# Optimization experiments

Measured on AMD Instinct MI355X. Metric: run time of the kernel, lower is better.

The kernel has to match this reference:

```python
import jax, jax.numpy as jnp
import numpy as np

B, C, HW, NP, L, D, NH, OUT = 32, 3, 224, 14, 12, 768, 12, 1000
PS = HW // NP            # 16
IN_D = C * PS * PS       # 768
S = NP * NP + 1          # 197
DH = D // NH             # 64
MD = 4 * D               # 3072


def setup_inputs() -> dict:
    key = jax.random.key(0)
    ks = iter(jax.random.split(key, 32))
    g = lambda shape: jax.random.normal(next(ks), shape, dtype=jnp.float32) * 0.02
    return {
        "images": jax.random.normal(next(ks), (B, C, HW, HW), dtype=jnp.float32),
        "Wp": g((D, IN_D)), "bp": jnp.zeros((D,), jnp.float32),
        "cls": jax.random.normal(next(ks), (1, D), dtype=jnp.float32),
        "pos": jnp.zeros((S, D), jnp.float32),  # frozen zeros in original
        "ln1_g": jnp.ones((L, D), jnp.float32), "ln1_b": jnp.zeros((L, D), jnp.float32),
        "Wq": g((L, NH, DH, DH)), "bq": jnp.zeros((L, NH, DH), jnp.float32),
        "Wk": g((L, NH, DH, DH)), "bk": jnp.zeros((L, NH, DH), jnp.float32),
        "Wv": g((L, NH, DH, DH)), "bv": jnp.zeros((L, NH, DH), jnp.float32),
        "ln2_g": jnp.ones((L, D), jnp.float32), "ln2_b": jnp.zeros((L, D), jnp.float32),
        "W1": g((L, MD, D)), "b1": jnp.zeros((L, MD), jnp.float32),
        "W2": g((L, D, MD)), "b2": jnp.zeros((L, D), jnp.float32),
        "Wh": g((OUT, D)), "bh": jnp.zeros((OUT,), jnp.float32),
    }


def _layernorm(x, g, b, eps=1e-5):
    m = jnp.mean(x, axis=-1, keepdims=True)
    v = jnp.var(x, axis=-1, keepdims=True)
    return (x - m) * jax.lax.rsqrt(v + eps) * g + b


def reference(images, Wp, bp, cls, pos, ln1_g, ln1_b, Wq, bq, Wk, bk, Wv, bv,
              ln2_g, ln2_b, W1, b1, W2, b2, Wh, bh):
    n = images.shape[0]
    # patchify: flatten order is (c, ph, pw) per patch, matching torch .flatten()
    p = images.reshape(n, C, NP, PS, NP, PS).transpose(0, 2, 4, 1, 3, 5)
    p = p.reshape(n, NP * NP, IN_D)
    tokens = p @ Wp.T + bp                                    # [B, NP^2, D]
    tokens = jnp.concatenate([jnp.broadcast_to(cls, (n, 1, D)), tokens], axis=1)
    x = tokens + pos                                          # [B, S, D]

    scale = 1.0 / np.sqrt(DH)

    def block(x, prm):
        g1, b1n, wq, bqv, wk, bkv, wv, bvv, g2, b2n, w1, b1v, w2, b2v = prm
        h = _layernorm(x, g1, b1n)
        hh = h.reshape(n, S, NH, DH)                          # split heads
        q = jnp.einsum('bshd,hed->bshe', hh, wq) + bqv
        k = jnp.einsum('bshd,hed->bshe', hh, wk) + bkv
        v = jnp.einsum('bshd,hed->bshe', hh, wv) + bvv
        att = jax.nn.softmax(jnp.einsum('bqhe,bkhe->bhqk', q, k) * scale, axis=-1)
        o = jnp.einsum('bhqk,bkhe->bqhe', att, v).reshape(n, S, D)
        x = x + o
        h2 = _layernorm(x, g2, b2n)
        m = jax.nn.gelu(h2 @ w1.T + b1v, approximate=False) @ w2.T + b2v
        return x + m, None

    x, _ = jax.lax.scan(block, x,
                        (ln1_g, ln1_b, Wq, bq, Wk, bk, Wv, bv,
                         ln2_g, ln2_b, W1, b1, W2, b2))
    logits = x[:, 0] @ Wh.T + bh
    return jax.nn.softmax(logits, axis=-1)
```

## Files before the change

kernel.cpp:

```cpp
#include <hip/hip_runtime.h>
#include <math.h>
#include <stdint.h>

#define NBATCH 32
#define SEQ 197
#define DIM 768
#define NHEAD 12
#define DH 64
#define MDIM 3072
#define NLAYER 12
#define NPATCH 196
#define NOUT 1000
#define MROWS (NBATCH * SEQ)
#define SPLITK 2

typedef __bf16 bf16x8 __attribute__((ext_vector_type(8)));
typedef float f32x4 __attribute__((ext_vector_type(4)));

__device__ __forceinline__ unsigned short f2bf(float f) {
    unsigned u = __float_as_uint(f);
    unsigned r = u + 0x7fffu + ((u >> 16) & 1u);
    return (unsigned short)(r >> 16);
}

__device__ __forceinline__ f32x4 mfma16(bf16x8 a, bf16x8 b, f32x4 c) {
    return __builtin_amdgcn_mfma_f32_16x16x32_bf16(a, b, c, 0, 0, 0);
}

__device__ __forceinline__ void gload_lds16(const void* g, const void* lds) {
    __builtin_amdgcn_global_load_lds(
        (const __attribute__((address_space(1))) void*)(uintptr_t)g,
        (__attribute__((address_space(3))) void*)(uint32_t)(uintptr_t)lds,
        16, 0, 0);
}

#define WAIT_VMCNT_4() asm volatile("s_waitcnt vmcnt(4)" ::: "memory")
#define WAIT_VMCNT_0() asm volatile("s_waitcnt vmcnt(0)" ::: "memory")
#define BARRIER_RAW()                      \
    do {                                   \
        asm volatile("" ::: "memory");     \
        __builtin_amdgcn_s_barrier();      \
        asm volatile("" ::: "memory");     \
    } while (0)

__global__ __launch_bounds__(256) void cvt4(const float* __restrict__ src,
                                            unsigned short* __restrict__ dst, int n4) {
    int stride = gridDim.x * 256;
    for (int i = blockIdx.x * 256 + threadIdx.x; i < n4; i += stride) {
        float4 f = *(const float4*)(src + (size_t)i * 4);
        ushort4 o;
        o.x = f2bf(f.x); o.y = f2bf(f.y); o.z = f2bf(f.z); o.w = f2bf(f.w);
        *(ushort4*)(dst + (size_t)i * 4) = o;
    }
}

__global__ __launch_bounds__(256) void cvt_qkvw(const float* __restrict__ Wq,
                                                const float* __restrict__ Wk,
                                                const float* __restrict__ Wv,
                                                unsigned short* __restrict__ dst) {
    const int n = NLAYER * NHEAD * 3 * 64 * 64;
    int stride = gridDim.x * 256;
    for (int i = blockIdx.x * 256 + threadIdx.x; i < n; i += stride) {
        int d = i & 63, e = (i >> 6) & 63;
        int v = i >> 12;
        int t = v % 3, hh = (v / 3) % NHEAD, l = v / (3 * NHEAD);
        const float* src = (t == 0) ? Wq : (t == 1) ? Wk : Wv;
        dst[i] = f2bf(src[(((size_t)(l * NHEAD + hh)) * 64 + e) * 64 + d]);
    }
}

__global__ __launch_bounds__(256) void cls_pos_kernel(const float* __restrict__ cls,
                                                      const float* __restrict__ pos,
                                                      float* __restrict__ x) {
    int b = blockIdx.x, tid = threadIdx.x;
#pragma unroll
    for (int i = 0; i < 3; i++) {
        int c = tid + i * 256;
        x[(size_t)b * SEQ * DIM + c] = cls[c] + pos[c];
    }
}

__global__ __launch_bounds__(256) void gemm_patch_bf(const unsigned short* __restrict__ imgbf,
                                                     const unsigned short* __restrict__ wpbf,
                                                     const float* __restrict__ bp,
                                                     const float* __restrict__ pos,
                                                     float* __restrict__ x) {
    __shared__ __align__(16) unsigned short As[2][128 * 32];
    __shared__ __align__(16) unsigned short Bs[2][128 * 32];
    const int t = threadIdx.x, l = t & 63, w = t >> 6;
    const int bm = blockIdx.x * 128, bn = blockIdx.y * 128;
    const int wr = w >> 1, wc = w & 1;
    f32x4 acc[4][4] = {};

    const int ra0 = t >> 2, ka0 = (t & 3) * 8;
    const int ra1 = (t + 256) >> 2, ka1 = ((t + 256) & 3) * 8;
    int gm0 = bm + ra0, b0 = gm0 / NPATCH, p0 = gm0 % NPATCH;
    int gm1 = bm + ra1, b1 = gm1 / NPATCH, p1 = gm1 % NPATCH;
    const unsigned short* ib0 =
        imgbf + ((size_t)b0 * 3 * 224 + (size_t)(p0 / 14) * 16) * 224 + (p0 % 14) * 16;
    const unsigned short* ib1 =
        imgbf + ((size_t)b1 * 3 * 224 + (size_t)(p1 / 14) * 16) * 224 + (p1 % 14) * 16;
    const unsigned short* Br0 = wpbf + (size_t)(bn + ra0) * 768 + ka0;
    const unsigned short* Br1 = wpbf + (size_t)(bn + ra1) * 768 + ka1;
    const int lA0 = (0 * 256 + w * 64) * 8, lA1 = (1 * 256 + w * 64) * 8;
    const int lr = l & 15, lk = (l >> 4) * 8;

#define PATCH_STAGE(buf, k0)                                                   \
    {                                                                          \
        int kA0 = (k0) + ka0, kA1 = (k0) + ka1;                                \
        int c0 = kA0 >> 8, i0 = (kA0 >> 4) & 15, j0 = kA0 & 15;                \
        int c1 = kA1 >> 8, i1 = (kA1 >> 4) & 15, j1 = kA1 & 15;                \
        gload_lds16(ib0 + ((size_t)c0 * 224 + i0) * 224 + j0, As[buf] + lA0);  \
        gload_lds16(ib1 + ((size_t)c1 * 224 + i1) * 224 + j1, As[buf] + lA1);  \
        gload_lds16(Br0 + (k0), Bs[buf] + lA0);                                \
        gload_lds16(Br1 + (k0), Bs[buf] + lA1);                                \
    }

    PATCH_STAGE(0, 0);
    int cur = 0;
    for (int k0 = 0; k0 < 768; k0 += 32) {
        if (k0 + 32 < 768) {
            PATCH_STAGE(cur ^ 1, k0 + 32);
            WAIT_VMCNT_4();
        } else {
            WAIT_VMCNT_0();
        }
        BARRIER_RAW();
        bf16x8 a[4], bfr[4];
#pragma unroll
        for (int m = 0; m < 4; m++)
            a[m] = *(const bf16x8*)(As[cur] + (wr * 64 + m * 16 + lr) * 32 + lk);
#pragma unroll
        for (int n = 0; n < 4; n++)
            bfr[n] = *(const bf16x8*)(Bs[cur] + (wc * 64 + n * 16 + lr) * 32 + lk);
#pragma unroll
        for (int m = 0; m < 4; m++)
#pragma unroll
            for (int n = 0; n < 4; n++)
                acc[m][n] = mfma16(a[m], bfr[n], acc[m][n]);
        BARRIER_RAW();
        cur ^= 1;
    }
#undef PATCH_STAGE

#pragma unroll
    for (int m = 0; m < 4; m++) {
#pragma unroll
        for (int r = 0; r < 4; r++) {
            int gm = bm + wr * 64 + m * 16 + (l >> 4) * 4 + r;
            int b2 = gm / NPATCH, p2 = gm % NPATCH;
            size_t orow = (size_t)(b2 * SEQ + 1 + p2) * DIM;
#pragma unroll
            for (int n = 0; n < 4; n++) {
                int gn = bn + wc * 64 + n * 16 + lr;
                x[orow + gn] = acc[m][n][r] + bp[gn] + pos[(size_t)(1 + p2) * DIM + gn];
            }
        }
    }
}

template <int RES, int RED>
__global__ __launch_bounds__(256) void ln_wave(const float* __restrict__ x_in,
                                               const float* __restrict__ addv,
                                               float* __restrict__ x_out,
                                               unsigned short* __restrict__ h_out,
                                               const float* __restrict__ g,
                                               const float* __restrict__ bb,
                                               const float* __restrict__ parts,
                                               const float* __restrict__ badd,
                                               int xmul) {
    int w = threadIdx.x >> 6, l = threadIdx.x & 63;
    size_t row = (size_t)blockIdx.x * 4 + w;
    size_t xrow = row * xmul;
    const float* xr = x_in + xrow * DIM;
    float4 v[3];
    float s = 0.f;
#pragma unroll
    for (int u = 0; u < 3; u++) {
        int c = u * 256 + l * 4;
        v[u] = *(const float4*)(xr + c);
        if (RES) {
            float4 a4 = *(const float4*)(addv + xrow * DIM + c);
            v[u].x += a4.x; v[u].y += a4.y; v[u].z += a4.z; v[u].w += a4.w;
        }
        if (RED) {
            float4 b4 = *(const float4*)(badd + c);
            v[u].x += b4.x; v[u].y += b4.y; v[u].z += b4.z; v[u].w += b4.w;
#pragma unroll
            for (int kc = 0; kc < SPLITK; kc++) {
                float4 p4 = *(const float4*)(parts + ((size_t)kc * MROWS + row) * DIM + c);
                v[u].x += p4.x; v[u].y += p4.y; v[u].z += p4.z; v[u].w += p4.w;
            }
        }
        s += v[u].x + v[u].y + v[u].z + v[u].w;
    }
#pragma unroll
    for (int o = 1; o < 64; o <<= 1) s += __shfl_xor(s, o, 64);
    float mean = s * (1.0f / 768.0f);
    float s2 = 0.f;
#pragma unroll
    for (int u = 0; u < 3; u++) {
        float dx = v[u].x - mean, dy = v[u].y - mean, dz = v[u].z - mean, dw = v[u].w - mean;
        s2 += dx * dx + dy * dy + dz * dz + dw * dw;
    }
#pragma unroll
    for (int o = 1; o < 64; o <<= 1) s2 += __shfl_xor(s2, o, 64);
    float inv = rsqrtf(s2 * (1.0f / 768.0f) + 1e-5f);
#pragma unroll
    for (int u = 0; u < 3; u++) {
        int c = u * 256 + l * 4;
        float4 g4 = *(const float4*)(g + c);
        float4 b4 = *(const float4*)(bb + c);
        ushort4 o;
        o.x = f2bf((v[u].x - mean) * inv * g4.x + b4.x);
        o.y = f2bf((v[u].y - mean) * inv * g4.y + b4.y);
        o.z = f2bf((v[u].z - mean) * inv * g4.z + b4.z);
        o.w = f2bf((v[u].w - mean) * inv * g4.w + b4.w);
        *(ushort4*)(h_out + row * DIM + c) = o;
        if (RES || RED) *(float4*)(x_out + xrow * DIM + c) = v[u];
    }
}

#define KS_OFF 0
#define QS_OFF 14400
#define VT_OFF 28800
#define RG_OFF 43648
#define WS_OFF (RG_OFF + 14400)

template <int QTMAX>
__global__ __launch_bounds__(512) void fused_attn(const unsigned short* __restrict__ hbf,
                                                  const unsigned short* __restrict__ wqkv,
                                                  const float* __restrict__ bq,
                                                  const float* __restrict__ bk,
                                                  const float* __restrict__ bv,
                                                  float* __restrict__ o) {
    __shared__ __align__(16) unsigned short lds[73344];
    const int b = blockIdx.x, hd = blockIdx.y;
    const int t = threadIdx.x, l = t & 63, w = t >> 6;
    const size_t base = ((size_t)b * SEQ) * DIM + hd * DH;
    const int lr = l & 15, lk4 = l >> 4;
    const unsigned short* wh = wqkv + (size_t)hd * 12288;

    for (int i = t; i < 197 * 16; i += 512) {
        int s = i >> 4, c4 = i & 15;
        ushort4 v4 = *(const ushort4*)(hbf + base + (size_t)s * DIM + c4 * 4);
        *(ushort4*)(lds + RG_OFF + s * 72 + c4 * 4) = v4;
    }
    if (t < 48) {
        int s = 197 + (t >> 4), c4 = t & 15;
        ushort4 z; z.x = 0; z.y = 0; z.z = 0; z.w = 0;
        *(ushort4*)(lds + RG_OFF + s * 72 + c4 * 4) = z;
    }
    for (int i = t; i < 192 * 16; i += 512) {
        int r = i >> 4, c4 = i & 15;
        ushort4 v4 = *(const ushort4*)(wh + (size_t)r * 64 + c4 * 4);
        *(ushort4*)(lds + WS_OFF + r * 72 + c4 * 4) = v4;
    }
    for (int i = t; i < 64 * 32; i += 512) {
        int d = i >> 5, s2 = 197 + (i & 31);
        if (s2 < 232) lds[VT_OFF + d * 232 + s2] = 0;
    }
    __syncthreads();

    for (int st = w; st < 13; st += 8) {
        bf16x8 a0 = *(const bf16x8*)(lds + RG_OFF + (st * 16 + lr) * 72 + lk4 * 8);
        bf16x8 a1 = *(const bf16x8*)(lds + RG_OFF + (st * 16 + lr) * 72 + 32 + lk4 * 8);
#pragma unroll
        for (int tt = 0; tt < 3; tt++) {
            if (QTMAX == 1 && tt == 0 && st >= QTMAX) continue;
            const float* bias = (tt == 0) ? bq : (tt == 1) ? bk : bv;
#pragma unroll
            for (int et = 0; et < 4; et++) {
                int wrow = (tt * 64 + et * 16 + lr) * 72;
                bf16x8 b0 = *(const bf16x8*)(lds + WS_OFF + wrow + lk4 * 8);
                bf16x8 b1 = *(const bf16x8*)(lds + WS_OFF + wrow + 32 + lk4 * 8);
                f32x4 acc = {0.f, 0.f, 0.f, 0.f};
                acc = mfma16(a0, b0, acc);
                acc = mfma16(a1, b1, acc);
                int e = et * 16 + lr;
                float bval = bias[hd * 64 + e];
#pragma unroll
                for (int r = 0; r < 4; r++) {
                    int s = st * 16 + lk4 * 4 + r;
                    if (s < SEQ) {
                        unsigned short val = f2bf(acc[r] + bval);
                        if (tt == 0) lds[QS_OFF + s * 72 + e] = val;
                        else if (tt == 1) lds[KS_OFF + s * 72 + e] = val;
                        else lds[VT_OFF + e * 232 + s] = val;
                    }
                }
            }
        }
    }
    __syncthreads();

    const int Pb = RG_OFF + w * 3712;
    {
        int jj = 208 + lk4 * 4;
        lds[Pb + lr * 232 + jj + 0] = 0;
        lds[Pb + lr * 232 + jj + 1] = 0;
        lds[Pb + lr * 232 + jj + 2] = 0;
        lds[Pb + lr * 232 + jj + 3] = 0;
    }

    for (int qt = w; qt < QTMAX; qt += 8) {
        int qrow = min(qt * 16 + lr, SEQ - 1);
        bf16x8 q0 = *(const bf16x8*)(lds + QS_OFF + qrow * 72 + lk4 * 8);
        bf16x8 q1 = *(const bf16x8*)(lds + QS_OFF + qrow * 72 + 32 + lk4 * 8);
        f32x4 st_[13];
#pragma unroll
        for (int jt = 0; jt < 13; jt++) st_[jt] = (f32x4){0.f, 0.f, 0.f, 0.f};
#pragma unroll
        for (int jt = 0; jt < 13; jt++) {
            int jrow = min(jt * 16 + lr, SEQ - 1);
            bf16x8 k0 = *(const bf16x8*)(lds + KS_OFF + jrow * 72 + lk4 * 8);
            bf16x8 k1 = *(const bf16x8*)(lds + KS_OFF + jrow * 72 + 32 + lk4 * 8);
            st_[jt] = mfma16(k0, q0, st_[jt]);
            st_[jt] = mfma16(k1, q1, st_[jt]);
        }
        float mx = -1e30f;
#pragma unroll
        for (int jt = 0; jt < 13; jt++)
#pragma unroll
            for (int r = 0; r < 4; r++) {
                int j = jt * 16 + lk4 * 4 + r;
                float sv = st_[jt][r] * 0.125f;
                st_[jt][r] = (j < SEQ) ? sv : -1e30f;
                mx = fmaxf(mx, st_[jt][r]);
            }
        mx = fmaxf(mx, __shfl_xor(mx, 16, 64));
        mx = fmaxf(mx, __shfl_xor(mx, 32, 64));
        float sum = 0.f;
#pragma unroll
        for (int jt = 0; jt < 13; jt++)
#pragma unroll
            for (int r = 0; r < 4; r++) {
                float p = __expf(st_[jt][r] - mx);
                st_[jt][r] = p;
                sum += p;
            }
        sum += __shfl_xor(sum, 16, 64);
        sum += __shfl_xor(sum, 32, 64);
        float inv = 1.0f / sum;
#pragma unroll
        for (int jt = 0; jt < 13; jt++) {
            ushort4 pk;
            pk.x = f2bf(st_[jt][0] * inv); pk.y = f2bf(st_[jt][1] * inv);
            pk.z = f2bf(st_[jt][2] * inv); pk.w = f2bf(st_[jt][3] * inv);
            *(ushort4*)(lds + Pb + lr * 232 + jt * 16 + lk4 * 4) = pk;
        }
        f32x4 acc[4] = {};
#pragma unroll
        for (int kt = 0; kt < 7; kt++) {
            bf16x8 pa = *(const bf16x8*)(lds + Pb + lr * 232 + kt * 32 + lk4 * 8);
#pragma unroll
            for (int nt = 0; nt < 4; nt++) {
                bf16x8 bv8 = *(const bf16x8*)(lds + VT_OFF + (nt * 16 + lr) * 232 + kt * 32 + lk4 * 8);
                acc[nt] = mfma16(pa, bv8, acc[nt]);
            }
        }
#pragma unroll
        for (int nt = 0; nt < 4; nt++)
#pragma unroll
            for (int r = 0; r < 4; r++) {
                int qq = qt * 16 + lk4 * 4 + r;
                if (qq < SEQ) o[base + (size_t)qq * DIM + nt * 16 + lr] = acc[nt][r];
            }
    }
}

template <int MODE, int SWAPXY>
__global__ __launch_bounds__(256) void gemm_bf(const unsigned short* __restrict__ A,
                                               const unsigned short* __restrict__ Bw,
                                               const float* __restrict__ bias,
                                               void* __restrict__ Cout,
                                               const float* __restrict__ res,
                                               int M, int N, int K) {
    __shared__ __align__(16) unsigned short As[2][128 * 32];
    __shared__ __align__(16) unsigned short Bs[2][128 * 32];
    const int t = threadIdx.x, l = t & 63, w = t >> 6;
    const int bm = (SWAPXY ? blockIdx.y : blockIdx.x) * 128;
    const int bn = (SWAPXY ? blockIdx.x : blockIdx.y) * 128;
    const int wr = w >> 1, wc = w & 1;
    f32x4 acc[4][4] = {};

    const int ra0 = t >> 2, ka0 = (t & 3) * 8;
    const int ra1 = (t + 256) >> 2, ka1 = ((t + 256) & 3) * 8;
    const unsigned short* Ar0 = A + (size_t)min(bm + ra0, M - 1) * K + ka0;
    const unsigned short* Ar1 = A + (size_t)min(bm + ra1, M - 1) * K + ka1;
    const unsigned short* Br0 = Bw + (size_t)(bn + ra0) * K + ka0;
    const unsigned short* Br1 = Bw + (size_t)(bn + ra1) * K + ka1;
    const int lo0 = (0 * 256 + w * 64) * 8, lo1 = (1 * 256 + w * 64) * 8;
    const int lr = l & 15, lk = (l >> 4) * 8;

    gload_lds16(Ar0, As[0] + lo0);
    gload_lds16(Ar1, As[0] + lo1);
    gload_lds16(Br0, Bs[0] + lo0);
    gload_lds16(Br1, Bs[0] + lo1);
    int cur = 0;
    for (int k0 = 0; k0 < K; k0 += 32) {
        if (k0 + 32 < K) {
            gload_lds16(Ar0 + k0 + 32, As[cur ^ 1] + lo0);
            gload_lds16(Ar1 + k0 + 32, As[cur ^ 1] + lo1);
            gload_lds16(Br0 + k0 + 32, Bs[cur ^ 1] + lo0);
            gload_lds16(Br1 + k0 + 32, Bs[cur ^ 1] + lo1);
            WAIT_VMCNT_4();
        } else {
            WAIT_VMCNT_0();
        }
        BARRIER_RAW();
        bf16x8 a[4], bfr[4];
#pragma unroll
        for (int m = 0; m < 4; m++)
            a[m] = *(const bf16x8*)(As[cur] + (wr * 64 + m * 16 + lr) * 32 + lk);
#pragma unroll
        for (int n = 0; n < 4; n++)
            bfr[n] = *(const bf16x8*)(Bs[cur] + (wc * 64 + n * 16 + lr) * 32 + lk);
#pragma unroll
        for (int m = 0; m < 4; m++)
#pragma unroll
            for (int n = 0; n < 4; n++)
                acc[m][n] = mfma16(a[m], bfr[n], acc[m][n]);
        BARRIER_RAW();
        cur ^= 1;
    }

#pragma unroll
    for (int m = 0; m < 4; m++) {
#pragma unroll
        for (int r = 0; r < 4; r++) {
            int gm = bm + wr * 64 + m * 16 + (l >> 4) * 4 + r;
            if (gm >= M) continue;
#pragma unroll
            for (int n = 0; n < 4; n++) {
                int gn = bn + wc * 64 + n * 16 + lr;
                float vb = acc[m][n][r] + bias[gn];
                if (MODE == 1) {
                    float gl = 0.5f * vb * (1.0f + erff(vb * 0.70710678118f));
                    ((unsigned short*)Cout)[(size_t)gm * N + gn] = f2bf(gl);
                } else {
                    ((float*)Cout)[(size_t)gm * N + gn] = vb + res[(size_t)gm * N + gn];
                }
            }
        }
    }
}

__global__ __launch_bounds__(256) void gemm_splitk(const unsigned short* __restrict__ A,
                                                   const unsigned short* __restrict__ Bw,
                                                   float* __restrict__ parts,
                                                   int M, int N, int KFULL) {
    __shared__ __align__(16) unsigned short As[2][128 * 32];
    __shared__ __align__(16) unsigned short Bs[2][128 * 32];
    const int t = threadIdx.x, l = t & 63, w = t >> 6;
    const int bm = blockIdx.x * 128, bn = blockIdx.y * 128;
    const int KC = KFULL / SPLITK;
    const int kbeg = blockIdx.z * KC;
    const int wr = w >> 1, wc = w & 1;
    f32x4 acc[4][4] = {};

    const int ra0 = t >> 2, ka0 = (t & 3) * 8;
    const int ra1 = (t + 256) >> 2, ka1 = ((t + 256) & 3) * 8;
    const unsigned short* Ar0 = A + (size_t)min(bm + ra0, M - 1) * KFULL + kbeg + ka0;
    const unsigned short* Ar1 = A + (size_t)min(bm + ra1, M - 1) * KFULL + kbeg + ka1;
    const unsigned short* Br0 = Bw + (size_t)(bn + ra0) * KFULL + kbeg + ka0;
    const unsigned short* Br1 = Bw + (size_t)(bn + ra1) * KFULL + kbeg + ka1;
    const int lo0 = (0 * 256 + w * 64) * 8, lo1 = (1 * 256 + w * 64) * 8;
    const int lr = l & 15, lk = (l >> 4) * 8;

    gload_lds16(Ar0, As[0] + lo0);
    gload_lds16(Ar1, As[0] + lo1);
    gload_lds16(Br0, Bs[0] + lo0);
    gload_lds16(Br1, Bs[0] + lo1);
    int cur = 0;
    for (int k0 = 0; k0 < KC; k0 += 32) {
        if (k0 + 32 < KC) {
            gload_lds16(Ar0 + k0 + 32, As[cur ^ 1] + lo0);
            gload_lds16(Ar1 + k0 + 32, As[cur ^ 1] + lo1);
            gload_lds16(Br0 + k0 + 32, Bs[cur ^ 1] + lo0);
            gload_lds16(Br1 + k0 + 32, Bs[cur ^ 1] + lo1);
            WAIT_VMCNT_4();
        } else {
            WAIT_VMCNT_0();
        }
        BARRIER_RAW();
        bf16x8 a[4], bfr[4];
#pragma unroll
        for (int m = 0; m < 4; m++)
            a[m] = *(const bf16x8*)(As[cur] + (wr * 64 + m * 16 + lr) * 32 + lk);
#pragma unroll
        for (int n = 0; n < 4; n++)
            bfr[n] = *(const bf16x8*)(Bs[cur] + (wc * 64 + n * 16 + lr) * 32 + lk);
#pragma unroll
        for (int m = 0; m < 4; m++)
#pragma unroll
            for (int n = 0; n < 4; n++)
                acc[m][n] = mfma16(a[m], bfr[n], acc[m][n]);
        BARRIER_RAW();
        cur ^= 1;
    }

    float* po = parts + (size_t)blockIdx.z * M * N;
#pragma unroll
    for (int m = 0; m < 4; m++) {
#pragma unroll
        for (int r = 0; r < 4; r++) {
            int gm = bm + wr * 64 + m * 16 + (l >> 4) * 4 + r;
            if (gm >= M) continue;
#pragma unroll
            for (int n = 0; n < 4; n++) {
                int gn = bn + wc * 64 + n * 16 + lr;
                po[(size_t)gm * N + gn] = acc[m][n][r];
            }
        }
    }
}

__global__ __launch_bounds__(256) void head_kernel(const float* __restrict__ x,
                                                   const float* __restrict__ Wh,
                                                   const float* __restrict__ bh,
                                                   float* __restrict__ logits,
                                                   const float* __restrict__ cparts,
                                                   const float* __restrict__ b2l) {
    __shared__ float xs[768];
    int b = blockIdx.x;
    int tid = threadIdx.x;
#pragma unroll
    for (int i = 0; i < 3; i++) {
        int c = tid + i * 256;
        float v = x[(size_t)b * SEQ * DIM + c];
        if (cparts) {
            v += b2l[c];
            v += cparts[(size_t)b * DIM + c];
            v += cparts[(size_t)NBATCH * DIM + (size_t)b * DIM + c];
        }
        xs[c] = v;
    }
    __syncthreads();
    int wave = tid >> 6, lane = tid & 63;
    int o = blockIdx.y * 4 + wave;
    if (o < NOUT) {
        float acc = 0;
#pragma unroll
        for (int t = 0; t < 12; t++) {
            int d = lane + t * 64;
            acc = fmaf(xs[d], Wh[(size_t)o * DIM + d], acc);
        }
#pragma unroll
        for (int off = 32; off > 0; off >>= 1) acc += __shfl_down(acc, off, 64);
        if (lane == 0) logits[b * NOUT + o] = acc + bh[o];
    }
}

__global__ __launch_bounds__(256) void softmax_kernel(const float* __restrict__ logits,
                                                      float* __restrict__ out) {
    __shared__ float tmp[4];
    int b = blockIdx.x, tid = threadIdx.x;
    float vals[4];
    float mx = -1e30f;
#pragma unroll
    for (int i = 0; i < 4; i++) {
        int c = tid + i * 256;
        vals[i] = (c < NOUT) ? logits[b * NOUT + c] : -1e30f;
        mx = fmaxf(mx, vals[i]);
    }
#pragma unroll
    for (int o = 32; o > 0; o >>= 1) mx = fmaxf(mx, __shfl_down(mx, o, 64));
    int wave = tid >> 6, lane = tid & 63;
    __syncthreads();
    if (lane == 0) tmp[wave] = mx;
    __syncthreads();
    mx = fmaxf(fmaxf(tmp[0], tmp[1]), fmaxf(tmp[2], tmp[3]));
    float s = 0;
#pragma unroll
    for (int i = 0; i < 4; i++) {
        int c = tid + i * 256;
        if (c < NOUT) {
            vals[i] = __expf(vals[i] - mx);
            s += vals[i];
        } else vals[i] = 0.f;
    }
#pragma unroll
    for (int o = 32; o > 0; o >>= 1) s += __shfl_down(s, o, 64);
    __syncthreads();
    if (lane == 0) tmp[wave] = s;
    __syncthreads();
    s = tmp[0] + tmp[1] + tmp[2] + tmp[3];
    float invs = 1.0f / s;
#pragma unroll
    for (int i = 0; i < 4; i++) {
        int c = tid + i * 256;
        if (c < NOUT) out[b * NOUT + c] = vals[i] * invs;
    }
}

extern "C" void kernel_launch(void* const* d_in, const int* in_sizes, int n_in,
                              void* d_out, int out_size, void* d_ws, size_t ws_size,
                              hipStream_t stream) {
    const float* images = (const float*)d_in[0];
    const float* Wp   = (const float*)d_in[1];
    const float* bp   = (const float*)d_in[2];
    const float* cls  = (const float*)d_in[3];
    const float* pos  = (const float*)d_in[4];
    const float* ln1g = (const float*)d_in[5];
    const float* ln1b = (const float*)d_in[6];
    const float* Wq   = (const float*)d_in[7];
    const float* bq   = (const float*)d_in[8];
    const float* Wk   = (const float*)d_in[9];
    const float* bk   = (const float*)d_in[10];
    const float* Wv   = (const float*)d_in[11];
    const float* bv   = (const float*)d_in[12];
    const float* ln2g = (const float*)d_in[13];
    const float* ln2b = (const float*)d_in[14];
    const float* W1   = (const float*)d_in[15];
    const float* b1   = (const float*)d_in[16];
    const float* W2   = (const float*)d_in[17];
    const float* b2   = (const float*)d_in[18];
    const float* Wh   = (const float*)d_in[19];
    const float* bh   = (const float*)d_in[20];
    float* out = (float*)d_out;

    const size_t NX = (size_t)MROWS * DIM;
    const size_t NIMG = (size_t)NBATCH * 3 * 224 * 224;
    const size_t NW = (size_t)MDIM * DIM;

    char* p = (char*)d_ws;
    float* x      = (float*)p;            p += NX * 4;
    float* h      = (float*)p;            p += NX * 4;
    float* logits = (float*)p;            p += (size_t)NBATCH * NOUT * 4;
    unsigned short* hbf   = (unsigned short*)p; p += NX * 2;
    unsigned short* h2bf  = (unsigned short*)p; p += NX * 2;
    unsigned short* mid   = (unsigned short*)p; p += (size_t)MROWS * MDIM * 2;
    unsigned short* wqkvb = (unsigned short*)p; p += (size_t)NLAYER * NHEAD * 12288 * 2;
    unsigned short* imgbf = (unsigned short*)p; p += NIMG * 2;
    unsigned short* wpbf  = (unsigned short*)p; p += (size_t)DIM * DIM * 2;

    size_t used = (size_t)(p - (char*)d_ws);
    bool skq = ws_size >= used + (size_t)SPLITK * NX * 4;
    float* parts = (float*)p;
    if (skq) p += (size_t)SPLITK * NX * 4;
    used = (size_t)(p - (char*)d_ws);
    bool big = ws_size >= used + (size_t)2 * NLAYER * NW * 2;
    unsigned short* w1a = (unsigned short*)p;
    unsigned short* w2a = big ? w1a + (size_t)NLAYER * NW : w1a + NW;

    cls_pos_kernel<<<dim3(NBATCH), dim3(256), 0, stream>>>(cls, pos, x);
    cvt4<<<dim3(2048), dim3(256), 0, stream>>>(images, imgbf, (int)(NIMG / 4));
    cvt4<<<dim3(576), dim3(256), 0, stream>>>(Wp, wpbf, (int)(DIM * DIM / 4));
    cvt_qkvw<<<dim3(1024), dim3(256), 0, stream>>>(Wq, Wk, Wv, wqkvb);
    gemm_patch_bf<<<dim3(49, 6), dim3(256), 0, stream>>>(imgbf, wpbf, bp, pos, x);
    if (big) {
        cvt4<<<dim3(2048), dim3(256), 0, stream>>>(W1, w1a, (int)(NLAYER * NW / 4));
        cvt4<<<dim3(2048), dim3(256), 0, stream>>>(W2, w2a, (int)(NLAYER * NW / 4));
    }

    for (int l = 0; l < NLAYER; l++) {
        const unsigned short* wl1 = big ? w1a + (size_t)l * NW : w1a;
        const unsigned short* wl2 = big ? w2a + (size_t)l * NW : w2a;
        if (!big) {
            cvt4<<<dim3(2048), dim3(256), 0, stream>>>(W1 + (size_t)l * NW, w1a, (int)(NW / 4));
            cvt4<<<dim3(2048), dim3(256), 0, stream>>>(W2 + (size_t)l * NW, w1a + NW, (int)(NW / 4));
        }
        if (skq && l > 0) {
            ln_wave<0, 1><<<dim3(MROWS / 4), dim3(256), 0, stream>>>(
                x, nullptr, x, hbf, ln1g + l * DIM, ln1b + l * DIM, parts, b2 + (l - 1) * DIM, 1);
        } else {
            ln_wave<0, 0><<<dim3(MROWS / 4), dim3(256), 0, stream>>>(
                x, nullptr, nullptr, hbf, ln1g + l * DIM, ln1b + l * DIM, nullptr, nullptr, 1);
        }
        bool last = skq && (l == NLAYER - 1);
        if (last) {
            fused_attn<1><<<dim3(NBATCH, NHEAD), dim3(512), 0, stream>>>(
                hbf, wqkvb + (size_t)l * NHEAD * 12288,
                bq + l * NHEAD * DH, bk + l * NHEAD * DH, bv + l * NHEAD * DH, h);
            ln_wave<1, 0><<<dim3(NBATCH / 4), dim3(256), 0, stream>>>(
                x, h, x, h2bf, ln2g + l * DIM, ln2b + l * DIM, nullptr, nullptr, SEQ);
            gemm_bf<1, 1><<<dim3(24, 1), dim3(256), 0, stream>>>(
                h2bf, wl1, b1 + l * MDIM, mid, nullptr, NBATCH, MDIM, DIM);
            gemm_splitk<<<dim3(1, 6, SPLITK), dim3(256), 0, stream>>>(
                mid, wl2, parts, NBATCH, DIM, MDIM);
        } else {
            fused_attn<13><<<dim3(NBATCH, NHEAD), dim3(512), 0, stream>>>(
                hbf, wqkvb + (size_t)l * NHEAD * 12288,
                bq + l * NHEAD * DH, bk + l * NHEAD * DH, bv + l * NHEAD * DH, h);
            ln_wave<1, 0><<<dim3(MROWS / 4), dim3(256), 0, stream>>>(
                x, h, x, h2bf, ln2g + l * DIM, ln2b + l * DIM, nullptr, nullptr, 1);
            gemm_bf<1, 1><<<dim3(24, 50), dim3(256), 0, stream>>>(
                h2bf, wl1, b1 + l * MDIM, mid, nullptr, MROWS, MDIM, DIM);
            if (skq) {
                gemm_splitk<<<dim3(50, 6, SPLITK), dim3(256), 0, stream>>>(
                    mid, wl2, parts, MROWS, DIM, MDIM);
            } else {
                gemm_bf<2, 0><<<dim3(50, 6), dim3(256), 0, stream>>>(
                    mid, wl2, b2 + l * DIM, x, x, MROWS, DIM, MDIM);
            }
        }
    }

    head_kernel<<<dim3(NBATCH, 250), dim3(256), 0, stream>>>(
        x, Wh, bh, logits,
        skq ? parts : nullptr, skq ? b2 + (NLAYER - 1) * DIM : nullptr);
    softmax_kernel<<<dim3(NBATCH), dim3(256), 0, stream>>>(logits, out);
}
```

Measured before the change: 2.152 ms.

## Replace MLP GEMMs with 256x256 eight-wave pipelined kernel and split-K of four

Adds a 512-thread GEMM kernel with 256x256 output tiles, 64-wide K steps, XOR-swizzled LDS, quadrant-interleaved staging and MFMA priority hints. It replaces both the FC1 (GELU) and the split-K FC2 GEMMs on the skq path. SPLITK rises to 4 so the FC2 launch still fills the device with the larger tiles, and the partial-sum consumers now loop over SPLITK. The goal is more data reuse per block and better overlap of loads with MFMA. The cost is extra partial-sum traffic and fewer blocks per GEMM. Padded tiles waste work on M=6304 and on the tiny last-layer case.

```diff
diff --git a/kernel.cpp b/kernel.cpp
--- a/kernel.cpp
+++ b/kernel.cpp
@@ -12,7 +12,7 @@
 #define NPATCH 196
 #define NOUT 1000
 #define MROWS (NBATCH * SEQ)
-#define SPLITK 2
+#define SPLITK 4
 
 typedef __bf16 bf16x8 __attribute__((ext_vector_type(8)));
 typedef float f32x4 __attribute__((ext_vector_type(4)));
@@ -369,6 +369,127 @@
     }
 }
 
+template <int MODE>
+__global__ __launch_bounds__(512) void gemm8p(const unsigned short* __restrict__ A,
+                                              const unsigned short* __restrict__ Bw,
+                                              const float* __restrict__ bias,
+                                              unsigned short* __restrict__ Cbf,
+                                              float* __restrict__ parts,
+                                              int M, int N, int lda, int ldb) {
+    __shared__ __align__(16) unsigned short As[2][2][8192];
+    __shared__ __align__(16) unsigned short Bs[2][2][8192];
+    const int t = threadIdx.x, l = t & 63, w = t >> 6;
+    const int bn = blockIdx.x * 256, bm = blockIdx.y * 256;
+    const int kbase = (MODE == 3) ? blockIdx.z * 768 : 0;
+    const int wr2 = w >> 2, wc2 = w & 3;
+    const int lr = l & 15, lk4 = l >> 4;
+    f32x4 acc[8][4] = {};
+
+    const int srow = t >> 3;
+    const int scol = (((t & 7) ^ ((t >> 3) & 7)) << 3);
+    const int ldst = w * 512;
+
+#define STAGE_A(kt, h, slot)                                                        \
+    do {                                                                            \
+        _Pragma("unroll") for (int i = 0; i < 2; i++) {                             \
+            int ra = min(bm + (h)*128 + i * 64 + srow, M - 1);                      \
+            gload_lds16(A + (size_t)ra * lda + kbase + (kt)*64 + scol,              \
+                        &As[slot][h][i * 4096 + ldst]);                             \
+        }                                                                           \
+    } while (0)
+#define STAGE_B(kt, h, slot)                                                        \
+    do {                                                                            \
+        _Pragma("unroll") for (int i = 0; i < 2; i++) {                             \
+            int rb = bn + (h)*128 + i * 64 + srow;                                  \
+            gload_lds16(Bw + (size_t)rb * ldb + kbase + (kt)*64 + scol,             \
+                        &Bs[slot][h][i * 4096 + ldst]);                             \
+        }                                                                           \
+    } while (0)
+
+    STAGE_A(0, 0, 0); STAGE_A(0, 1, 0); STAGE_B(0, 0, 0); STAGE_B(0, 1, 0);
+    STAGE_B(1, 0, 1); STAGE_A(1, 1, 1);
+
+    for (int it = 0; it < 6; ++it) {
+#pragma unroll
+        for (int p = 0; p < 8; p++) {
+            {
+                const int sofs = (p <= 1) ? 1 : (p <= 5 ? 2 : 3);
+                const int skt = 2 * it + sofs;
+                const int sslot = skt & 1;
+                if (skt < 12) {
+                    if (p == 0)      STAGE_A(skt, 0, sslot);
+                    else if (p == 1) STAGE_B(skt, 1, sslot);
+                    else if (p == 2) STAGE_B(skt, 0, sslot);
+                    else if (p == 3) STAGE_A(skt, 1, sslot);
+                    else if (p == 4) STAGE_A(skt, 0, sslot);
+                    else if (p == 5) STAGE_B(skt, 1, sslot);
+                    else if (p == 6) STAGE_B(skt, 0, sslot);
+                    else             STAGE_A(skt, 1, sslot);
+                }
+            }
+            WAIT_VMCNT_4();
+            BARRIER_RAW();
+            const int slot = p >> 2;
+            const int q = p & 3;
+            const int MQ = (q == 1 || q == 2) ? 1 : 0;
+            const int NQ = (q >= 2) ? 1 : 0;
+            bf16x8 af[4][2], bfv[2][2];
+#pragma unroll
+            for (int mf = 0; mf < 4; mf++) {
+                int lrow = wr2 * 64 + mf * 16 + lr;
+                int sw = (lrow & 7) << 4;
+#pragma unroll
+                for (int kk = 0; kk < 2; kk++)
+                    af[mf][kk] = *(const bf16x8*)((const char*)As[slot][MQ] + lrow * 128 +
+                                                  ((kk * 64 + lk4 * 16) ^ sw));
+            }
+#pragma unroll
+            for (int nf = 0; nf < 2; nf++) {
+                int lrow = wc2 * 32 + nf * 16 + lr;
+                int sw = (lrow & 7) << 4;
+#pragma unroll
+                for (int kk = 0; kk < 2; kk++)
+                    bfv[nf][kk] = *(const bf16x8*)((const char*)Bs[slot][NQ] + lrow * 128 +
+                                                   ((kk * 64 + lk4 * 16) ^ sw));
+            }
+            __builtin_amdgcn_s_setprio(1);
+#pragma unroll
+            for (int kk = 0; kk < 2; kk++)
+#pragma unroll
+                for (int mf = 0; mf < 4; mf++)
+#pragma unroll
+                    for (int nf = 0; nf < 2; nf++)
+                        acc[MQ * 4 + mf][NQ * 2 + nf] =
+                            mfma16(af[mf][kk], bfv[nf][kk], acc[MQ * 4 + mf][NQ * 2 + nf]);
+            __builtin_amdgcn_s_setprio(0);
+            BARRIER_RAW();
+        }
+    }
+#undef STAGE_A
+#undef STAGE_B
+
+    float* po = (MODE == 3) ? parts + (size_t)blockIdx.z * M * N : nullptr;
+#pragma unroll
+    for (int mi = 0; mi < 8; mi++) {
+#pragma unroll
+        for (int r = 0; r < 4; r++) {
+            int gm = bm + (mi >> 2) * 128 + wr2 * 64 + (mi & 3) * 16 + lk4 * 4 + r;
+            if (gm >= M) continue;
+#pragma unroll
+            for (int ni = 0; ni < 4; ni++) {
+                int gn = bn + (ni >> 1) * 128 + wc2 * 32 + (ni & 1) * 16 + lr;
+                if (MODE == 1) {
+                    float vb = acc[mi][ni][r] + bias[gn];
+                    float gl = 0.5f * vb * (1.0f + erff(vb * 0.70710678118f));
+                    Cbf[(size_t)gm * N + gn] = f2bf(gl);
+                } else {
+                    po[(size_t)gm * N + gn] = acc[mi][ni][r];
+                }
+            }
+        }
+    }
+}
+
 template <int MODE, int SWAPXY>
 __global__ __launch_bounds__(256) void gemm_bf(const unsigned short* __restrict__ A,
                                                const unsigned short* __restrict__ Bw,
@@ -446,76 +567,6 @@
     }
 }
 
-__global__ __launch_bounds__(256) void gemm_splitk(const unsigned short* __restrict__ A,
-                                                   const unsigned short* __restrict__ Bw,
-                                                   float* __restrict__ parts,
-                                                   int M, int N, int KFULL) {
-    __shared__ __align__(16) unsigned short As[2][128 * 32];
-    __shared__ __align__(16) unsigned short Bs[2][128 * 32];
-    const int t = threadIdx.x, l = t & 63, w = t >> 6;
-    const int bm = blockIdx.x * 128, bn = blockIdx.y * 128;
-    const int KC = KFULL / SPLITK;
-    const int kbeg = blockIdx.z * KC;
-    const int wr = w >> 1, wc = w & 1;
-    f32x4 acc[4][4] = {};
-
-    const int ra0 = t >> 2, ka0 = (t & 3) * 8;
-    const int ra1 = (t + 256) >> 2, ka1 = ((t + 256) & 3) * 8;
-    const unsigned short* Ar0 = A + (size_t)min(bm + ra0, M - 1) * KFULL + kbeg + ka0;
-    const unsigned short* Ar1 = A + (size_t)min(bm + ra1, M - 1) * KFULL + kbeg + ka1;
-    const unsigned short* Br0 = Bw + (size_t)(bn + ra0) * KFULL + kbeg + ka0;
-    const unsigned short* Br1 = Bw + (size_t)(bn + ra1) * KFULL + kbeg + ka1;
-    const int lo0 = (0 * 256 + w * 64) * 8, lo1 = (1 * 256 + w * 64) * 8;
-    const int lr = l & 15, lk = (l >> 4) * 8;
-
-    gload_lds16(Ar0, As[0] + lo0);
-    gload_lds16(Ar1, As[0] + lo1);
-    gload_lds16(Br0, Bs[0] + lo0);
-    gload_lds16(Br1, Bs[0] + lo1);
-    int cur = 0;
-    for (int k0 = 0; k0 < KC; k0 += 32) {
-        if (k0 + 32 < KC) {
-            gload_lds16(Ar0 + k0 + 32, As[cur ^ 1] + lo0);
-            gload_lds16(Ar1 + k0 + 32, As[cur ^ 1] + lo1);
-            gload_lds16(Br0 + k0 + 32, Bs[cur ^ 1] + lo0);
-            gload_lds16(Br1 + k0 + 32, Bs[cur ^ 1] + lo1);
-            WAIT_VMCNT_4();
-        } else {
-            WAIT_VMCNT_0();
-        }
-        BARRIER_RAW();
-        bf16x8 a[4], bfr[4];
-#pragma unroll
-        for (int m = 0; m < 4; m++)
-            a[m] = *(const bf16x8*)(As[cur] + (wr * 64 + m * 16 + lr) * 32 + lk);
-#pragma unroll
-        for (int n = 0; n < 4; n++)
-            bfr[n] = *(const bf16x8*)(Bs[cur] + (wc * 64 + n * 16 + lr) * 32 + lk);
-#pragma unroll
-        for (int m = 0; m < 4; m++)
-#pragma unroll
-            for (int n = 0; n < 4; n++)
-                acc[m][n] = mfma16(a[m], bfr[n], acc[m][n]);
-        BARRIER_RAW();
-        cur ^= 1;
-    }
-
-    float* po = parts + (size_t)blockIdx.z * M * N;
-#pragma unroll
-    for (int m = 0; m < 4; m++) {
-#pragma unroll
-        for (int r = 0; r < 4; r++) {
-            int gm = bm + wr * 64 + m * 16 + (l >> 4) * 4 + r;
-            if (gm >= M) continue;
-#pragma unroll
-            for (int n = 0; n < 4; n++) {
-                int gn = bn + wc * 64 + n * 16 + lr;
-                po[(size_t)gm * N + gn] = acc[m][n][r];
-            }
-        }
-    }
-}
-
 __global__ __launch_bounds__(256) void head_kernel(const float* __restrict__ x,
                                                    const float* __restrict__ Wh,
                                                    const float* __restrict__ bh,
@@ -531,8 +582,9 @@
         float v = x[(size_t)b * SEQ * DIM + c];
         if (cparts) {
             v += b2l[c];
-            v += cparts[(size_t)b * DIM + c];
-            v += cparts[(size_t)NBATCH * DIM + (size_t)b * DIM + c];
+#pragma unroll
+            for (int kc = 0; kc < SPLITK; kc++)
+                v += cparts[((size_t)kc * NBATCH + b) * DIM + c];
         }
         xs[c] = v;
     }
@@ -675,22 +727,24 @@
                 bq + l * NHEAD * DH, bk + l * NHEAD * DH, bv + l * NHEAD * DH, h);
             ln_wave<1, 0><<<dim3(NBATCH / 4), dim3(256), 0, stream>>>(
                 x, h, x, h2bf, ln2g + l * DIM, ln2b + l * DIM, nullptr, nullptr, SEQ);
-            gemm_bf<1, 1><<<dim3(24, 1), dim3(256), 0, stream>>>(
-                h2bf, wl1, b1 + l * MDIM, mid, nullptr, NBATCH, MDIM, DIM);
-            gemm_splitk<<<dim3(1, 6, SPLITK), dim3(256), 0, stream>>>(
-                mid, wl2, parts, NBATCH, DIM, MDIM);
+            gemm8p<1><<<dim3(12, 1), dim3(512), 0, stream>>>(
+                h2bf, wl1, b1 + l * MDIM, mid, nullptr, NBATCH, MDIM, DIM, DIM);
+            gemm8p<3><<<dim3(3, 1, SPLITK), dim3(512), 0, stream>>>(
+                mid, wl2, nullptr, nullptr, parts, NBATCH, DIM, MDIM, MDIM);
         } else {
             fused_attn<13><<<dim3(NBATCH, NHEAD), dim3(512), 0, stream>>>(
                 hbf, wqkvb + (size_t)l * NHEAD * 12288,
                 bq + l * NHEAD * DH, bk + l * NHEAD * DH, bv + l * NHEAD * DH, h);
             ln_wave<1, 0><<<dim3(MROWS / 4), dim3(256), 0, stream>>>(
                 x, h, x, h2bf, ln2g + l * DIM, ln2b + l * DIM, nullptr, nullptr, 1);
-            gemm_bf<1, 1><<<dim3(24, 50), dim3(256), 0, stream>>>(
-                h2bf, wl1, b1 + l * MDIM, mid, nullptr, MROWS, MDIM, DIM);
             if (skq) {
-                gemm_splitk<<<dim3(50, 6, SPLITK), dim3(256), 0, stream>>>(
-                    mid, wl2, parts, MROWS, DIM, MDIM);
+                gemm8p<1><<<dim3(12, 25), dim3(512), 0, stream>>>(
+                    h2bf, wl1, b1 + l * MDIM, mid, nullptr, MROWS, MDIM, DIM, DIM);
+                gemm8p<3><<<dim3(3, 25, SPLITK), dim3(512), 0, stream>>>(
+                    mid, wl2, nullptr, nullptr, parts, MROWS, DIM, MDIM, MDIM);
             } else {
+                gemm_bf<1, 1><<<dim3(24, 50), dim3(256), 0, stream>>>(
+                    h2bf, wl1, b1 + l * MDIM, mid, nullptr, MROWS, MDIM, DIM);
                 gemm_bf<2, 0><<<dim3(50, 6), dim3(256), 0, stream>>>(
                     mid, wl2, b2 + l * DIM, x, x, MROWS, DIM, MDIM);
             }
```

Result: slower. 2.542 ms (+18.1%).
